# Optimization experiments

Measured on AMD Instinct MI355X. Metric: run time of the kernel, lower is better.

The kernel has to match this reference:

```python
import jax, jax.numpy as jnp
import numpy as np

NUM_EMBEDDINGS = 8192
EMBEDDING_DIM = 512
COMMITMENT_COST = 0.1


def setup_inputs() -> dict:
    key = jax.random.key(0)
    k_z, k_cb = jax.random.split(key)
    z = jax.random.normal(k_z, (16, 1024, EMBEDDING_DIM), dtype=jnp.float32)
    # nn.Embedding weight init: uniform(-1/num_embeddings, 1/num_embeddings)
    bound = 1.0 / NUM_EMBEDDINGS
    codebook = jax.random.uniform(
        k_cb, (NUM_EMBEDDINGS, EMBEDDING_DIM), dtype=jnp.float32,
        minval=-bound, maxval=bound)
    return {"z": z, "codebook": codebook}


def reference(z, codebook):
    # z: [B, T, D], codebook: [K, D]
    zf = z.reshape(-1, z.shape[-1])                      # [N, D]
    # squared euclidean distances: ||z||^2 + ||e||^2 - 2 z e^T  -> [N, K]
    distances = (jnp.sum(zf * zf, axis=1, keepdims=True)
                 + jnp.sum(codebook * codebook, axis=1)
                 - 2.0 * jnp.matmul(zf, codebook.T))
    indices = jnp.argmin(distances, axis=1)              # [N]
    z_quantized = codebook[indices].reshape(z.shape)     # [B, T, D]
    zq_sg = jax.lax.stop_gradient(z_quantized)
    commitment_loss = jnp.mean((zq_sg - z) ** 2)
    # mse(z, zq.detach()) == mse(zq.detach(), z) == commitment_loss
    vq_loss = commitment_loss + COMMITMENT_COST * commitment_loss
    # straight-through estimator
    z_st = z + jax.lax.stop_gradient(z_quantized - z)
    return (z_st, vq_loss)
```

## Files before the change

kernel.cpp:

```cpp
#include <hip/hip_runtime.h>


#define M_ROWS 16384
#define K_CODES 8192
#define DIM 512
#define BM 128
#define BN 128
#define BK 128
#define NT (K_CODES / BN)
#define OUT0_SIZE (M_ROWS * DIM)
#define GB_BLOCKS 1024

typedef int   i32x8 __attribute__((ext_vector_type(8)));
typedef float f32x4 __attribute__((ext_vector_type(4)));

template <bool HI>
__device__ __forceinline__ int pk8(float a, float b, int old) {
    return __builtin_amdgcn_cvt_pk_fp8_f32(a, b, old, HI);
}

__global__ __launch_bounds__(256) void convert_all(
    const float* __restrict__ z, const float* __restrict__ cb,
    unsigned char* __restrict__ z8, unsigned char* __restrict__ cb8,
    float* __restrict__ enorm, float* __restrict__ lossSlot)
{
    const int tid = threadIdx.x;
    if (blockIdx.x < K_CODES / 4) {
        const int w = tid >> 6, lane = tid & 63;
        const int row = blockIdx.x * 4 + w;
        const float* src = cb + (size_t)row * DIM + lane * 8;
        float4 a = *(const float4*)(src);
        float4 b = *(const float4*)(src + 4);
        float ns = a.x * a.x + a.y * a.y + a.z * a.z + a.w * a.w
                 + b.x * b.x + b.y * b.y + b.z * b.z + b.w * b.w;
        const float S = 8192.0f;
        int lo = 0, hi = 0;
        lo = pk8<false>(a.x * S, a.y * S, lo); lo = pk8<true>(a.z * S, a.w * S, lo);
        hi = pk8<false>(b.x * S, b.y * S, hi); hi = pk8<true>(b.z * S, b.w * S, hi);
        *(int2*)(cb8 + (size_t)row * DIM + lane * 8) = make_int2(lo, hi);
        for (int m = 32; m; m >>= 1) ns += __shfl_down(ns, m, 64);
        if (lane == 0) enorm[row] = S * ns;
        if (blockIdx.x == 0 && tid == 0) *lossSlot = 0.f;
    } else {
        size_t i = ((size_t)(blockIdx.x - K_CODES / 4) * 256 + tid) * 8;
        float4 a = *(const float4*)(z + i);
        float4 b = *(const float4*)(z + i + 4);
        int lo = 0, hi = 0;
        lo = pk8<false>(a.x, a.y, lo); lo = pk8<true>(a.z, a.w, lo);
        hi = pk8<false>(b.x, b.y, hi); hi = pk8<true>(b.z, b.w, hi);
        *(int2*)(z8 + i) = make_int2(lo, hi);
    }
}

__global__ __launch_bounds__(256, 2) void gemm_argmin(
    const unsigned char* __restrict__ z8, const unsigned char* __restrict__ cb8,
    const float* __restrict__ enorm, unsigned int* __restrict__ candV)
{
    __shared__ alignas(32) unsigned char As[BM * BK];
    __shared__ alignas(32) unsigned char Bs[BN * BK];
    __shared__ float Es[BN];
    __shared__ unsigned int cU[BM][2];

    const int tid = threadIdx.x;
    const int lane = tid & 63;
    const int w = tid >> 6;
    const int ktile = blockIdx.x;
    const int mtile = blockIdx.y;
    const int mbase = mtile * BM;
    const int nbase = ktile * BN;

    if (tid < BN) Es[tid] = enorm[nbase + tid];

    f32x4 acc[16];
#pragma unroll
    for (int i = 0; i < 16; ++i) acc[i] = (f32x4){0.f, 0.f, 0.f, 0.f};

    const int rA = lane >> 3;
    const int jG = ((lane & 7) ^ rA) * 16;
    const int quad = lane >> 4;
    const int l15 = lane & 15;
    const int sw = l15 & 7;
    const int rw = (w >> 1) * 64;
    const int cw = (w & 1) * 64;
    const int t32 = ((quad << 1) ^ (sw & 6)) * 16;

    for (int dt = 0; dt < DIM; dt += BK) {
#pragma unroll
        for (int i = 0; i < 4; ++i) {
            int c = w * 4 + i;
            int row = c * 8 + rA;
            const unsigned char* ga = z8 + (size_t)(mbase + row) * DIM + dt + jG;
            const unsigned char* gb = cb8 + (size_t)(nbase + row) * DIM + dt + jG;
            unsigned char* la = As + c * 1024 + lane * 16;
            unsigned char* lb = Bs + c * 1024 + lane * 16;
            __builtin_amdgcn_global_load_lds((const __attribute__((address_space(1))) void*)ga,
                                             (__attribute__((address_space(3))) void*)la, 16, 0, 0);
            __builtin_amdgcn_global_load_lds((const __attribute__((address_space(1))) void*)gb,
                                             (__attribute__((address_space(3))) void*)lb, 16, 0, 0);
        }
        __syncthreads();
        i32x8 bfr[4];
#pragma unroll
        for (int cf = 0; cf < 4; ++cf)
            bfr[cf] = *(const i32x8*)(Bs + (cw + cf * 16 + l15) * BK + t32);
#pragma unroll
        for (int rf = 0; rf < 4; ++rf) {
            i32x8 a = *(const i32x8*)(As + (rw + rf * 16 + l15) * BK + t32);
#pragma unroll
            for (int cf = 0; cf < 4; ++cf)
                acc[rf * 4 + cf] = __builtin_amdgcn_mfma_scale_f32_16x16x128_f8f6f4(
                    a, bfr[cf], acc[rf * 4 + cf],
                    0, 0,
                    0, 0x7F7F7F7F,
                    0, 0x7F7F7F7F);
        }
        __syncthreads();
    }

    float es[4];
#pragma unroll
    for (int cf = 0; cf < 4; ++cf) es[cf] = Es[cw + cf * 16 + l15];

#pragma unroll
    for (int rf = 0; rf < 4; ++rf) {
#pragma unroll
        for (int r = 0; r < 4; ++r) {
            float bv = 3.4e38f; int bi = 0;
#pragma unroll
            for (int cf = 0; cf < 4; ++cf) {
                int col = cw + cf * 16 + l15;
                float dist = fmaf(-2.0f, acc[rf * 4 + cf][r], es[cf]);
                if (dist < bv) { bv = dist; bi = col; }
            }
            unsigned u = __builtin_bit_cast(unsigned, bv);
            u ^= ((unsigned)(((int)u) >> 31)) | 0x80000000u;
            unsigned key = (u & 0xFFFFE000u) | (unsigned)(nbase + bi);
#pragma unroll
            for (int m = 1; m < 16; m <<= 1) {
                unsigned o = __shfl_xor(key, m, 64);
                key = o < key ? o : key;
            }
            if (l15 == 0) cU[rw + rf * 16 + quad * 4 + r][w & 1] = key;
        }
    }
    __syncthreads();
    if (tid < BM) {
        unsigned k0 = cU[tid][0], k1 = cU[tid][1];
        candV[(size_t)ktile * M_ROWS + mbase + tid] = k0 < k1 ? k0 : k1;
    }
}

__global__ __launch_bounds__(256) void gather_out(
    const float* __restrict__ z, const float* __restrict__ cb,
    const unsigned int* __restrict__ candV, float* __restrict__ out)
{
    __shared__ float red[4];
    const int tid = threadIdx.x;
    const int w = tid >> 6, lane = tid & 63;
    float lsum = 0.f;
#pragma unroll
    for (int it = 0; it < M_ROWS / (GB_BLOCKS * 4); ++it) {
        int row = (it * GB_BLOCKS + blockIdx.x) * 4 + w;
        unsigned key = candV[(size_t)lane * M_ROWS + row];
#pragma unroll
        for (int m = 1; m < 64; m <<= 1) {
            unsigned o = __shfl_xor(key, m, 64);
            key = o < key ? o : key;
        }
        int k = (int)(key & 8191u);
#pragma unroll
        for (int j = 0; j < 2; ++j) {
            int slot = lane + j * 64;
            float4 zv = ((const float4*)(z + (size_t)row * DIM))[slot];
            float4 cv = ((const float4*)(cb + (size_t)k * DIM))[slot];
            float dx = cv.x - zv.x, dy = cv.y - zv.y;
            float dz2 = cv.z - zv.z, dw = cv.w - zv.w;
            float4 o = {zv.x + dx, zv.y + dy, zv.z + dz2, zv.w + dw};
            ((float4*)(out + (size_t)row * DIM))[slot] = o;
            lsum += dx * dx + dy * dy + dz2 * dz2 + dw * dw;
        }
    }
    for (int m = 32; m; m >>= 1) lsum += __shfl_down(lsum, m, 64);
    if (lane == 0) red[w] = lsum;
    __syncthreads();
    if (tid == 0) {
        float t = (red[0] + red[1]) + (red[2] + red[3]);
        atomicAdd(out + OUT0_SIZE, t * (1.1f / (float)OUT0_SIZE));
    }
}

extern "C" void kernel_launch(void* const* d_in, const int* in_sizes, int n_in,
                              void* d_out, int out_size, void* d_ws, size_t ws_size,
                              hipStream_t stream) {
    const float* z = (const float*)d_in[0];
    const float* cb = (const float*)d_in[1];
    float* out = (float*)d_out;
    char* ws = (char*)d_ws;

    unsigned char* z8   = (unsigned char*)(ws);
    unsigned char* cb8  = (unsigned char*)(ws + 8388608);
    float* enorm        = (float*)(ws + 12582912);
    unsigned int* candV = (unsigned int*)(ws + 12615680);

    convert_all<<<K_CODES / 4 + M_ROWS * DIM / 2048, 256, 0, stream>>>(
        z, cb, z8, cb8, enorm, out + OUT0_SIZE);
    gemm_argmin<<<dim3(NT, M_ROWS / BM), 256, 0, stream>>>(z8, cb8, enorm, candV);
    gather_out<<<GB_BLOCKS, 256, 0, stream>>>(z, cb, candV, out);
}
```

Measured before the change: 270.1 us.

## Double-buffer GEMM LDS tiles, remap blocks per XCD, replace loss atomics with reduction

The fp8 GEMM-argmin kernel now double-buffers its A and B shared-memory tiles, so the global-to-LDS load for the next K slice is issued while the current slice is being multiplied. The grid is flattened and remapped so that consecutive blocks on each XCD share M tiles, aiming for better L2 reuse. The loss accumulation drops the per-block atomicAdd and its zeroing in favour of a per-block partials array plus a final single-block reduce kernel, which makes the sum deterministic at the cost of one extra launch. Doubling LDS to about 64KB per block may limit occupancy to two blocks per CU, and the loop still has one barrier per iteration.

```diff
diff --git a/kernel.cpp b/kernel.cpp
--- a/kernel.cpp
+++ b/kernel.cpp
@@ -22,7 +22,7 @@
 __global__ __launch_bounds__(256) void convert_all(
     const float* __restrict__ z, const float* __restrict__ cb,
     unsigned char* __restrict__ z8, unsigned char* __restrict__ cb8,
-    float* __restrict__ enorm, float* __restrict__ lossSlot)
+    float* __restrict__ enorm)
 {
     const int tid = threadIdx.x;
     if (blockIdx.x < K_CODES / 4) {
@@ -40,7 +40,6 @@
         *(int2*)(cb8 + (size_t)row * DIM + lane * 8) = make_int2(lo, hi);
         for (int m = 32; m; m >>= 1) ns += __shfl_down(ns, m, 64);
         if (lane == 0) enorm[row] = S * ns;
-        if (blockIdx.x == 0 && tid == 0) *lossSlot = 0.f;
     } else {
         size_t i = ((size_t)(blockIdx.x - K_CODES / 4) * 256 + tid) * 8;
         float4 a = *(const float4*)(z + i);
@@ -56,16 +55,19 @@
     const unsigned char* __restrict__ z8, const unsigned char* __restrict__ cb8,
     const float* __restrict__ enorm, unsigned int* __restrict__ candV)
 {
-    __shared__ alignas(32) unsigned char As[BM * BK];
-    __shared__ alignas(32) unsigned char Bs[BN * BK];
+    __shared__ alignas(32) unsigned char As[2][BM * BK];
+    __shared__ alignas(32) unsigned char Bs[2][BN * BK];
     __shared__ float Es[BN];
     __shared__ unsigned int cU[BM][2];
 
     const int tid = threadIdx.x;
     const int lane = tid & 63;
     const int w = tid >> 6;
-    const int ktile = blockIdx.x;
-    const int mtile = blockIdx.y;
+    const int phys = blockIdx.x;
+    const int xcd = phys & 7;
+    const int idx = phys >> 3;
+    const int ktile = idx >> 4;
+    const int mtile = xcd * 16 + (idx & 15);
     const int mbase = mtile * BM;
     const int nbase = ktile * BN;
 
@@ -84,28 +86,35 @@
     const int cw = (w & 1) * 64;
     const int t32 = ((quad << 1) ^ (sw & 6)) * 16;
 
-    for (int dt = 0; dt < DIM; dt += BK) {
-#pragma unroll
-        for (int i = 0; i < 4; ++i) {
-            int c = w * 4 + i;
-            int row = c * 8 + rA;
-            const unsigned char* ga = z8 + (size_t)(mbase + row) * DIM + dt + jG;
-            const unsigned char* gb = cb8 + (size_t)(nbase + row) * DIM + dt + jG;
-            unsigned char* la = As + c * 1024 + lane * 16;
-            unsigned char* lb = Bs + c * 1024 + lane * 16;
-            __builtin_amdgcn_global_load_lds((const __attribute__((address_space(1))) void*)ga,
-                                             (__attribute__((address_space(3))) void*)la, 16, 0, 0);
-            __builtin_amdgcn_global_load_lds((const __attribute__((address_space(1))) void*)gb,
-                                             (__attribute__((address_space(3))) void*)lb, 16, 0, 0);
-        }
-        __syncthreads();
+#define STAGE(buf, dt_) do {                                                  \
+    _Pragma("unroll")                                                         \
+    for (int i_ = 0; i_ < 4; ++i_) {                                          \
+        int c_ = w * 4 + i_;                                                  \
+        int row_ = c_ * 8 + rA;                                               \
+        const unsigned char* ga_ = z8 + (size_t)(mbase + row_) * DIM + (dt_) * BK + jG; \
+        const unsigned char* gb_ = cb8 + (size_t)(nbase + row_) * DIM + (dt_) * BK + jG; \
+        unsigned char* la_ = As[buf] + c_ * 1024 + lane * 16;                 \
+        unsigned char* lb_ = Bs[buf] + c_ * 1024 + lane * 16;                 \
+        __builtin_amdgcn_global_load_lds((const __attribute__((address_space(1))) void*)ga_, \
+                                         (__attribute__((address_space(3))) void*)la_, 16, 0, 0); \
+        __builtin_amdgcn_global_load_lds((const __attribute__((address_space(1))) void*)gb_, \
+                                         (__attribute__((address_space(3))) void*)lb_, 16, 0, 0); \
+    } } while (0)
+
+    STAGE(0, 0);
+    __syncthreads();
+
+#pragma unroll
+    for (int dt = 0; dt < 4; ++dt) {
+        const int cur = dt & 1;
+        if (dt < 3) STAGE(cur ^ 1, dt + 1);
         i32x8 bfr[4];
 #pragma unroll
         for (int cf = 0; cf < 4; ++cf)
-            bfr[cf] = *(const i32x8*)(Bs + (cw + cf * 16 + l15) * BK + t32);
+            bfr[cf] = *(const i32x8*)(Bs[cur] + (cw + cf * 16 + l15) * BK + t32);
 #pragma unroll
         for (int rf = 0; rf < 4; ++rf) {
-            i32x8 a = *(const i32x8*)(As + (rw + rf * 16 + l15) * BK + t32);
+            i32x8 a = *(const i32x8*)(As[cur] + (rw + rf * 16 + l15) * BK + t32);
 #pragma unroll
             for (int cf = 0; cf < 4; ++cf)
                 acc[rf * 4 + cf] = __builtin_amdgcn_mfma_scale_f32_16x16x128_f8f6f4(
@@ -116,6 +125,7 @@
         }
         __syncthreads();
     }
+#undef STAGE
 
     float es[4];
 #pragma unroll
@@ -152,7 +162,8 @@
 
 __global__ __launch_bounds__(256) void gather_out(
     const float* __restrict__ z, const float* __restrict__ cb,
-    const unsigned int* __restrict__ candV, float* __restrict__ out)
+    const unsigned int* __restrict__ candV, float* __restrict__ out,
+    float* __restrict__ partials)
 {
     __shared__ float red[4];
     const int tid = threadIdx.x;
@@ -183,10 +194,22 @@
     for (int m = 32; m; m >>= 1) lsum += __shfl_down(lsum, m, 64);
     if (lane == 0) red[w] = lsum;
     __syncthreads();
-    if (tid == 0) {
-        float t = (red[0] + red[1]) + (red[2] + red[3]);
-        atomicAdd(out + OUT0_SIZE, t * (1.1f / (float)OUT0_SIZE));
-    }
+    if (tid == 0) partials[blockIdx.x] = (red[0] + red[1]) + (red[2] + red[3]);
+}
+
+__global__ __launch_bounds__(256) void reduce_loss(
+    const float* __restrict__ partials, float* __restrict__ lossOut)
+{
+    __shared__ float red[4];
+    const int tid = threadIdx.x;
+    float s = 0.f;
+#pragma unroll
+    for (int i = 0; i < GB_BLOCKS / 256; ++i) s += partials[i * 256 + tid];
+    for (int m = 32; m; m >>= 1) s += __shfl_down(s, m, 64);
+    if ((tid & 63) == 0) red[tid >> 6] = s;
+    __syncthreads();
+    if (tid == 0)
+        lossOut[0] = ((red[0] + red[1]) + (red[2] + red[3])) * (1.1f / (float)OUT0_SIZE);
 }
 
 extern "C" void kernel_launch(void* const* d_in, const int* in_sizes, int n_in,
@@ -201,9 +224,11 @@
     unsigned char* cb8  = (unsigned char*)(ws + 8388608);
     float* enorm        = (float*)(ws + 12582912);
     unsigned int* candV = (unsigned int*)(ws + 12615680);
+    float* partials     = (float*)(ws + 16809984);
 
     convert_all<<<K_CODES / 4 + M_ROWS * DIM / 2048, 256, 0, stream>>>(
-        z, cb, z8, cb8, enorm, out + OUT0_SIZE);
-    gemm_argmin<<<dim3(NT, M_ROWS / BM), 256, 0, stream>>>(z8, cb8, enorm, candV);
-    gather_out<<<GB_BLOCKS, 256, 0, stream>>>(z, cb, candV, out);
-}
+        z, cb, z8, cb8, enorm);
+    gemm_argmin<<<NT * (M_ROWS / BM), 256, 0, stream>>>(z8, cb8, enorm, candV);
+    gather_out<<<GB_BLOCKS, 256, 0, stream>>>(z, cb, candV, out, partials);
+    reduce_loss<<<1, 256, 0, stream>>>(partials, out + OUT0_SIZE);
+}
```

Result: faster. 255.2 us (-5.5%).
